# Optimization experiments

Measured on AMD Instinct MI355X. Metric: run time of the kernel, lower is better.

## Reference

```python
import math
import jax, jax.numpy as jnp
import numpy as np

B, S, DIM, H = 16, 1024, 1024, 16
HD = DIM // H            # head_dim = 64
ROPE_DIM = HD // 2       # 32; per-axis rotary dim
FT = 32                  # ft_seq_len, FT*FT == S
PT = 16                  # pt_seq_len
THETA = 10000.0
EPS = 1e-6


def _rope_cos_sin():
    # freqs_for='lang'
    freqs = 1.0 / THETA ** (jnp.arange(0, ROPE_DIM, 2, dtype=jnp.float32) / ROPE_DIM)  # [ROPE_DIM//2]
    t = jnp.arange(FT, dtype=jnp.float32) / FT * PT                                    # [FT]
    fs = jnp.einsum('n,f->nf', t, freqs)                                               # [FT, ROPE_DIM//2]
    fs = jnp.repeat(fs, 2, axis=-1)                                                    # [FT, ROPE_DIM]
    fh = jnp.broadcast_to(fs[:, None, :], (FT, FT, ROPE_DIM))
    fw = jnp.broadcast_to(fs[None, :, :], (FT, FT, ROPE_DIM))
    f = jnp.concatenate([fh, fw], axis=-1).reshape(-1, 2 * ROPE_DIM)                   # [S, HD]
    return jnp.cos(f), jnp.sin(f)


def _rotate_half(x):
    x1, x2 = jnp.split(x, 2, axis=-1)
    return jnp.concatenate((-x2, x1), axis=-1)


def _rms_norm(x, w):
    xf = x.astype(jnp.float32)
    var = jnp.mean(jnp.square(xf), axis=-1, keepdims=True)
    return (w * (xf * jax.lax.rsqrt(var + EPS))).astype(x.dtype)


def setup_inputs() -> dict:
    key = jax.random.key(0)
    ks = jax.random.split(key, 4)
    sd = 1.0 / math.sqrt(DIM)
    return {
        'x': jax.random.normal(ks[0], (B, S, DIM), dtype=jnp.float32),
        'w_qkv': jax.random.normal(ks[1], (DIM, 3 * DIM), dtype=jnp.float32) * sd,
        'b_qkv': jnp.zeros((3 * DIM,), dtype=jnp.float32),
        'q_norm_w': jnp.ones((HD,), dtype=jnp.float32),
        'k_norm_w': jnp.ones((HD,), dtype=jnp.float32),
        'w_out': jax.random.normal(ks[2], (DIM, DIM), dtype=jnp.float32) * sd,
        'b_out': jnp.zeros((DIM,), dtype=jnp.float32),
    }


def reference(x, w_qkv, b_qkv, q_norm_w, k_norm_w, w_out, b_out):
    cos, sin = _rope_cos_sin()                    # [S, HD] each
    cos = cos[None, None].astype(x.dtype)
    sin = sin[None, None].astype(x.dtype)

    qkv = x @ w_qkv + b_qkv                       # [B,S,3*DIM]
    qkv = qkv.reshape(B, S, 3, H, HD).transpose(2, 0, 3, 1, 4)  # [3,B,H,S,HD]
    q, k, v = qkv[0], qkv[1], qkv[2]

    q = _rms_norm(q, q_norm_w)
    k = _rms_norm(k, k_norm_w)

    q = q * cos + _rotate_half(q) * sin
    k = k * cos + _rotate_half(k) * sin

    scale = 1.0 / math.sqrt(HD)
    logits = jnp.einsum('bhqd,bhkd->bhqk', q.astype(jnp.float32), k.astype(jnp.float32)) * scale
    attn = jax.nn.softmax(logits, axis=-1).astype(x.dtype)
    out = jnp.einsum('bhqk,bhkd->bhqd', attn, v)  # [B,H,S,HD]

    out = out.transpose(0, 2, 1, 3).reshape(B, S, DIM)
    return out @ w_out + b_out
```

## Files before the change

kernel.cpp:

```cpp
#include <hip/hip_runtime.h>
#include <cstdint>
#include <cstddef>

#define B_    16
#define S_    1024
#define DIM_  1024
#define H_    16
#define HD_   64
#define TDIM  3072

typedef unsigned short ushort_t;
typedef unsigned int   uint_t;
typedef __attribute__((ext_vector_type(8)))  short s8v;
typedef __attribute__((ext_vector_type(4)))  float f32x4;
typedef __attribute__((ext_vector_type(16))) float f32x16;

__device__ __forceinline__ float b2f(ushort_t u) {
    union { uint_t i; float f; } t; t.i = (uint_t)u << 16; return t.f;
}
__device__ __forceinline__ ushort_t f2b(float f) {
    union { float f; uint_t i; } t; t.f = f;
    uint_t r = t.i + 0x7FFFu + ((t.i >> 16) & 1u);
    return (ushort_t)(r >> 16);
}
__device__ __forceinline__ uint_t cvt_pk_bf16(float a, float b) {
    uint_t r;
    asm("v_cvt_pk_bf16_f32 %0, %1, %2" : "=v"(r) : "v"(a), "v"(b));
    return r;
}

__device__ __forceinline__ f32x4 mfma_bf16(s8v a, s8v b, f32x4 c) {
    asm volatile("v_mfma_f32_16x16x32_bf16 %0, %1, %2, %0" : "+v"(c) : "v"(a), "v"(b));
    return c;
}
__device__ __forceinline__ f32x16 mfma32_bf16(s8v a, s8v b, f32x16 c) {
    asm volatile("v_mfma_f32_32x32x16_bf16 %0, %1, %2, %0" : "+v"(c) : "v"(a), "v"(b));
    return c;
}

__device__ __forceinline__ void gload16(const void* g, void* l) {
    __builtin_amdgcn_global_load_lds(
        (const __attribute__((address_space(1))) uint_t*)g,
        (__attribute__((address_space(3))) uint_t*)l, 16, 0, 0);
}

__device__ __forceinline__ void bar() {
    asm volatile("" ::: "memory");
    __builtin_amdgcn_s_barrier();
    asm volatile("" ::: "memory");
}
__device__ __forceinline__ void wait_vm0() {
    asm volatile("s_waitcnt vmcnt(0)" ::: "memory");
}

__global__ __launch_bounds__(256) void f32_to_bf16_vec(const float* __restrict__ src,
                                                       short* __restrict__ dst, int n8) {
    int i = blockIdx.x * 256 + threadIdx.x;
    if (i < n8) {
        float4 a = *(const float4*)(src + (size_t)i * 8);
        float4 b = *(const float4*)(src + (size_t)i * 8 + 4);
        s8v t;
        t[0] = (short)f2b(a.x); t[1] = (short)f2b(a.y);
        t[2] = (short)f2b(a.z); t[3] = (short)f2b(a.w);
        t[4] = (short)f2b(b.x); t[5] = (short)f2b(b.y);
        t[6] = (short)f2b(b.z); t[7] = (short)f2b(b.w);
        *(s8v*)(dst + (size_t)i * 8) = t;
    }
}

__global__ __launch_bounds__(256) void rope_tables(float* __restrict__ cos_t,
                                                   float* __restrict__ sin_t) {
    int idx = blockIdx.x * 256 + threadIdx.x;
    int s = idx >> 6;
    int d = idx & 63;
    int pos = (d < 32) ? (s >> 5) : (s & 31);
    int i   = (d & 31) >> 1;
    float freq  = expf(-(float)i * 0.5756462732485115f);
    float angle = (float)pos * 0.5f * freq;
    cos_t[idx] = cosf(angle);
    sin_t[idx] = sinf(angle);
}

__global__ __launch_bounds__(256) void transpose_to_bf16(const float* __restrict__ Wsrc,
                                                         short* __restrict__ WT,
                                                         int K, int N) {
    __shared__ float t[32][33];
    int tx = threadIdx.x & 31, ty = threadIdx.x >> 5;
    int n0 = blockIdx.x * 32, k0 = blockIdx.y * 32;
#pragma unroll
    for (int i = 0; i < 4; ++i)
        t[ty + 8 * i][tx] = Wsrc[(size_t)(k0 + ty + 8 * i) * N + n0 + tx];
    __syncthreads();
#pragma unroll
    for (int i = 0; i < 4; ++i)
        WT[(size_t)(n0 + ty + 8 * i) * K + k0 + tx] = (short)f2b(t[tx][ty + 8 * i]);
}

template<typename CT, bool NORM>
__global__ __launch_bounds__(512, 2) void gemm8ph(
        const short* __restrict__ A, const short* __restrict__ BT,
        const float* __restrict__ bias, CT* __restrict__ C,
        int M, int N, int K, int NX,
        const float* __restrict__ qw, const float* __restrict__ kw,
        const float* __restrict__ cos_t, const float* __restrict__ sin_t) {
    __shared__ short As[2][256 * 64];
    __shared__ short Bs[2][256 * 64];

    const int tid  = threadIdx.x;
    const int w    = tid >> 6;
    const int lane = tid & 63;
    const int l15  = lane & 15, lg = lane >> 4;
    const int wm = w >> 2, wn = w & 3;

    const int nwg  = gridDim.x;
    const int cpx  = nwg >> 3;
    const int wgid = (blockIdx.x & 7) * cpx + (blockIdx.x >> 3);
    const int bx = wgid % NX, by = wgid / NX;
    const int m0 = by * 256, n0 = bx * 256;

    const int NT = K >> 6;

    const int sgrow = w * 8 + (lane >> 3);
    const int ksrc  = (((lane & 7) ^ (lane >> 3)) * 8);

    auto stageA = [&](int t, int buf) {
        const size_t k0 = (size_t)t * 64;
#pragma unroll
        for (int j = 0; j < 4; ++j)
            gload16(A + (size_t)(m0 + j * 64 + sgrow) * K + k0 + ksrc,
                    &As[buf][(j * 64 + w * 8) * 64]);
    };
    auto stageB = [&](int t, int buf) {
        const size_t k0 = (size_t)t * 64;
#pragma unroll
        for (int j = 0; j < 4; ++j)
            gload16(BT + (size_t)(n0 + j * 64 + sgrow) * K + k0 + ksrc,
                    &Bs[buf][(j * 64 + w * 8) * 64]);
    };

    stageA(0, 0);
    stageB(0, 0);
    wait_vm0();
    bar();

    f32x4 acc[8][4] = {};
    s8v a_f[4][2];
    s8v b_f[4][2];

    const int swz = l15 & 7;

    for (int t = 0; t < NT; ++t) {
        const int buf = t & 1;
        const bool more = (t + 1 < NT);

#pragma unroll
        for (int i = 0; i < 4; ++i) {
            int row = wm * 128 + i * 16 + l15;
#pragma unroll
            for (int kk = 0; kk < 2; ++kk)
                a_f[i][kk] = *(const s8v*)&As[buf][row * 64 + (((kk * 4 + lg) ^ swz) * 8)];
        }
#pragma unroll
        for (int ni = 0; ni < 2; ++ni) {
            int row = wn * 64 + ni * 16 + l15;
#pragma unroll
            for (int kk = 0; kk < 2; ++kk)
                b_f[ni][kk] = *(const s8v*)&Bs[buf][row * 64 + (((kk * 4 + lg) ^ swz) * 8)];
        }
        if (more) stageA(t + 1, buf ^ 1);
        bar();
        __builtin_amdgcn_s_setprio(1);
#pragma unroll
        for (int i = 0; i < 4; ++i)
#pragma unroll
            for (int ni = 0; ni < 2; ++ni)
#pragma unroll
                for (int kk = 0; kk < 2; ++kk)
                    acc[i][ni] = mfma_bf16(a_f[i][kk], b_f[ni][kk], acc[i][ni]);
        __builtin_amdgcn_s_setprio(0);
        bar();

#pragma unroll
        for (int ni = 2; ni < 4; ++ni) {
            int row = wn * 64 + ni * 16 + l15;
#pragma unroll
            for (int kk = 0; kk < 2; ++kk)
                b_f[ni][kk] = *(const s8v*)&Bs[buf][row * 64 + (((kk * 4 + lg) ^ swz) * 8)];
        }
        if (more) stageB(t + 1, buf ^ 1);
        bar();
        __builtin_amdgcn_s_setprio(1);
#pragma unroll
        for (int i = 0; i < 4; ++i)
#pragma unroll
            for (int ni = 2; ni < 4; ++ni)
#pragma unroll
                for (int kk = 0; kk < 2; ++kk)
                    acc[i][ni] = mfma_bf16(a_f[i][kk], b_f[ni][kk], acc[i][ni]);
        __builtin_amdgcn_s_setprio(0);
        bar();

#pragma unroll
        for (int i = 0; i < 4; ++i) {
            int row = wm * 128 + 64 + i * 16 + l15;
#pragma unroll
            for (int kk = 0; kk < 2; ++kk)
                a_f[i][kk] = *(const s8v*)&As[buf][row * 64 + (((kk * 4 + lg) ^ swz) * 8)];
        }
        bar();
        __builtin_amdgcn_s_setprio(1);
#pragma unroll
        for (int i = 0; i < 4; ++i)
#pragma unroll
            for (int ni = 0; ni < 2; ++ni)
#pragma unroll
                for (int kk = 0; kk < 2; ++kk)
                    acc[4 + i][ni] = mfma_bf16(a_f[i][kk], b_f[ni][kk], acc[4 + i][ni]);
        __builtin_amdgcn_s_setprio(0);
        bar();

        __builtin_amdgcn_s_setprio(1);
#pragma unroll
        for (int i = 0; i < 4; ++i)
#pragma unroll
            for (int ni = 2; ni < 4; ++ni)
#pragma unroll
                for (int kk = 0; kk < 2; ++kk)
                    acc[4 + i][ni] = mfma_bf16(a_f[i][kk], b_f[ni][kk], acc[4 + i][ni]);
        __builtin_amdgcn_s_setprio(0);
        wait_vm0();
        bar();
    }

    const int colbase = n0 + wn * 64;
    if constexpr (NORM) {
        if (colbase < 2048) {
            const float* nw = (colbase < 1024) ? qw : kw;
            float wv[4], bv[4];
#pragma unroll
            for (int ni = 0; ni < 4; ++ni) {
                wv[ni] = nw[16 * ni + l15];
                bv[ni] = bias[colbase + 16 * ni + l15];
            }
#pragma unroll
            for (int mi = 0; mi < 8; ++mi) {
#pragma unroll
                for (int r = 0; r < 4; ++r) {
                    int row = m0 + wm * 128 + mi * 16 + lg * 4 + r;
                    int s = row & (S_ - 1);
                    float v[4];
#pragma unroll
                    for (int ni = 0; ni < 4; ++ni) v[ni] = acc[mi][ni][r] + bv[ni];
                    float ss = v[0]*v[0] + v[1]*v[1] + v[2]*v[2] + v[3]*v[3];
                    ss += __shfl_xor(ss, 1);
                    ss += __shfl_xor(ss, 2);
                    ss += __shfl_xor(ss, 4);
                    ss += __shfl_xor(ss, 8);
                    float rms = rsqrtf(ss * (1.0f / 64.0f) + 1e-6f);
                    float xn[4];
#pragma unroll
                    for (int ni = 0; ni < 4; ++ni) xn[ni] = v[ni] * rms * wv[ni];
#pragma unroll
                    for (int ni = 0; ni < 4; ++ni) {
                        int d = 16 * ni + l15;
                        float c  = cos_t[s * 64 + d];
                        float sn = sin_t[s * 64 + d];
                        float rot = (ni < 2) ? -xn[ni + 2] : xn[ni - 2];
                        C[(size_t)row * N + colbase + d] = (short)f2b(xn[ni] * c + rot * sn);
                    }
                }
            }
            return;
        }
    }
#pragma unroll
    for (int ni = 0; ni < 4; ++ni) {
        float bvv = bias[colbase + 16 * ni + l15];
#pragma unroll
        for (int mi = 0; mi < 8; ++mi) {
#pragma unroll
            for (int r = 0; r < 4; ++r) {
                size_t row = (size_t)(m0 + wm * 128 + mi * 16 + lg * 4 + r);
                int    col = colbase + 16 * ni + l15;
                float v = acc[mi][ni][r] + bvv;
                if constexpr (sizeof(CT) == 4) C[row * N + col] = v;
                else                           C[row * N + col] = (short)f2b(v);
            }
        }
    }
}

__global__ __launch_bounds__(256) void attn_mfma(const short* __restrict__ qkv,
                                                 short* __restrict__ attn) {
    __shared__ ushort_t pool[9216];
    ushort_t* Ks = pool;
    ushort_t* Vt = pool + 4608;

    const float SC  = 0.18033688011112042f;
    const float THR = 11.0f;

    const int tid  = threadIdx.x;
    const int w    = tid >> 6;
    const int lane = tid & 63;
    const int l31  = lane & 31, l5 = lane >> 5;

    const int bid = blockIdx.x;
    const int xcd = bid & 7;
    const int jj_ = bid >> 3;
    const int bh  = xcd * 32 + (jj_ & 31);
    const int b   = bh >> 4, h = bh & 15;
    const int q0  = (jj_ >> 5) * 128;

    const short* qbase = qkv + (size_t)b * S_ * TDIM + h * HD_;
    const short* kb_ = qbase + DIM_;
    const short* vb_ = qbase + 2 * DIM_;

    s8v qf[4];
#pragma unroll
    for (int kc = 0; kc < 4; ++kc)
        qf[kc] = *(const s8v*)(qbase + (size_t)(q0 + w * 32 + l31) * TDIM + kc * 16 + l5 * 8);

    f32x16 of0 = {}, of1 = {};
    float m_s = -1e30f, l_s = 0.f;

    const int kr   = tid >> 3;
    const int kp8  = (tid & 7) * 8;
    const int vkp  = tid >> 3;
    const int va   = tid & 7;
    const int vp8  = va * 8;
    const int vcol = (2 * vkp) ^ ((va & 3) << 4);
    const int vsw  = ((l31 >> 3) & 3) << 4;

    s8v kA, kB, vA, vB;
    auto prefetch = [&](int kt) {
        const short* kbt = kb_ + (size_t)kt * 64 * TDIM;
        const short* vbt = vb_ + (size_t)kt * 64 * TDIM;
        kA = *(const s8v*)(kbt + (size_t)kr * TDIM + kp8);
        kB = *(const s8v*)(kbt + (size_t)(kr + 32) * TDIM + kp8);
        vA = *(const s8v*)(vbt + (size_t)(2 * vkp) * TDIM + vp8);
        vB = *(const s8v*)(vbt + (size_t)(2 * vkp + 1) * TDIM + vp8);
    };
    prefetch(0);

    for (int kt = 0; kt < 16; ++kt) {
        *(s8v*)&Ks[kr * 72 + kp8]        = kA;
        *(s8v*)&Ks[(kr + 32) * 72 + kp8] = kB;
#pragma unroll
        for (int j = 0; j < 8; ++j) {
            uint_t pk = (ushort_t)vA[j] | ((uint_t)(ushort_t)vB[j] << 16);
            *(uint_t*)&Vt[(vp8 + j) * 72 + vcol] = pk;
        }
        __syncthreads();

        if (kt < 15) prefetch(kt + 1);

        f32x16 st0 = {}, st1 = {};
        __builtin_amdgcn_s_setprio(1);
#pragma unroll
        for (int kc = 0; kc < 4; ++kc) {
            s8v kf0 = *(const s8v*)&Ks[l31 * 72 + kc * 16 + l5 * 8];
            s8v kf1 = *(const s8v*)&Ks[(32 + l31) * 72 + kc * 16 + l5 * 8];
            st0 = mfma32_bf16(kf0, qf[kc], st0);
            st1 = mfma32_bf16(kf1, qf[kc], st1);
        }
        __builtin_amdgcn_s_setprio(0);

        float mx = -1e30f;
#pragma unroll
        for (int r = 0; r < 16; ++r)
            mx = fmaxf(mx, fmaxf(st0[r], st1[r]));
        mx = fmaxf(mx, __shfl_xor(mx, 32));
        float mxs = mx * SC;

        if (!__all(mxs <= m_s + THR)) {
            float mnew  = fmaxf(m_s, mxs);
            float alpha = exp2f(m_s - mnew);
            m_s = mnew;
            l_s *= alpha;
#pragma unroll
            for (int r = 0; r < 16; ++r) { of0[r] *= alpha; of1[r] *= alpha; }
        }

        float ls = 0.f;
#pragma unroll
        for (int r = 0; r < 16; ++r) {
            float p0 = exp2f(__builtin_fmaf(st0[r], SC, -m_s));
            float p1 = exp2f(__builtin_fmaf(st1[r], SC, -m_s));
            st0[r] = p0; st1[r] = p1;
            ls += p0 + p1;
        }
        ls += __shfl_xor(ls, 32);
        l_s += ls;

        uint_t P20[8], P21[8];
#pragma unroll
        for (int i = 0; i < 8; ++i) {
            P20[i] = cvt_pk_bf16(st0[2 * i], st0[2 * i + 1]);
            P21[i] = cvt_pk_bf16(st1[2 * i], st1[2 * i + 1]);
        }

#pragma unroll
        for (int kb = 0; kb < 2; ++kb) {
            const uint_t* P2 = kb ? P21 : P20;
#pragma unroll
            for (int c = 0; c < 2; ++c) {
                uint_t sw0 = __shfl_xor((int)P2[4 * c + 0], 32);
                uint_t sw1 = __shfl_xor((int)P2[4 * c + 1], 32);
                uint_t sw2 = __shfl_xor((int)P2[4 * c + 2], 32);
                uint_t sw3 = __shfl_xor((int)P2[4 * c + 3], 32);
                union { uint_t u[4]; s8v v; } pf;
                pf.u[0] = l5 ? sw2           : P2[4 * c + 0];
                pf.u[1] = l5 ? sw3           : P2[4 * c + 1];
                pf.u[2] = l5 ? P2[4 * c + 2] : sw0;
                pf.u[3] = l5 ? P2[4 * c + 3] : sw1;

                int kcol = (kb * 32 + c * 16 + l5 * 8) ^ vsw;
                s8v vf0 = *(const s8v*)&Vt[l31 * 72 + kcol];
                s8v vf1 = *(const s8v*)&Vt[(32 + l31) * 72 + kcol];
                __builtin_amdgcn_s_setprio(1);
                of0 = mfma32_bf16(vf0, pf.v, of0);
                of1 = mfma32_bf16(vf1, pf.v, of1);
                __builtin_amdgcn_s_setprio(0);
            }
        }
        __syncthreads();
    }

    float inv = 1.0f / l_s;
    ushort_t* OL = pool + w * 2304;
#pragma unroll
    for (int r = 0; r < 16; ++r) {
        int d = (r & 3) + 8 * (r >> 2) + 4 * l5;
        OL[l31 * 72 + d]      = f2b(of0[r] * inv);
        OL[l31 * 72 + 32 + d] = f2b(of1[r] * inv);
    }
#pragma unroll
    for (int i = 0; i < 4; ++i) {
        int idx = lane + i * 64;
        int row = idx >> 3, ch = idx & 7;
        *(s8v*)&attn[((size_t)b * S_ + q0 + w * 32 + row) * DIM_ + h * HD_ + ch * 8] =
            *(const s8v*)&OL[row * 72 + ch * 8];
    }
}

extern "C" void kernel_launch(void* const* d_in, const int* in_sizes, int n_in,
                              void* d_out, int out_size, void* d_ws, size_t ws_size,
                              hipStream_t stream) {
    const float* x        = (const float*)d_in[0];
    const float* w_qkv    = (const float*)d_in[1];
    const float* b_qkv    = (const float*)d_in[2];
    const float* q_norm_w = (const float*)d_in[3];
    const float* k_norm_w = (const float*)d_in[4];
    const float* w_out    = (const float*)d_in[5];
    const float* b_out    = (const float*)d_in[6];
    float* out = (float*)d_out;

    const size_t OFF_QKV = 0;
    const size_t OFF_ATT = 100663296;
    const size_t OFF_XB  = OFF_ATT + 33554432;
    const size_t OFF_WQ  = OFF_XB + 33554432;
    const size_t OFF_WO  = OFF_WQ + 6291456;
    const size_t OFF_CT  = OFF_WO + 2097152;
    const size_t OFF_ST  = OFF_CT + 262144;
    const size_t NEED    = OFF_ST + 262144;

    if (ws_size < NEED) {
        hipMemsetAsync(d_out, 0, (size_t)out_size * sizeof(float), stream);
        return;
    }

    char* ws = (char*)d_ws;
    short* qkv   = (short*)(ws + OFF_QKV);
    short* attnb = (short*)(ws + OFF_ATT);
    short* xb    = (short*)(ws + OFF_XB);
    short* wqkvT = (short*)(ws + OFF_WQ);
    short* woutT = (short*)(ws + OFF_WO);
    float* cos_t = (float*)(ws + OFF_CT);
    float* sin_t = (float*)(ws + OFF_ST);

    rope_tables<<<dim3(256), dim3(256), 0, stream>>>(cos_t, sin_t);
    f32_to_bf16_vec<<<dim3(8192), dim3(256), 0, stream>>>(x, xb, 2097152);
    transpose_to_bf16<<<dim3(96, 32), dim3(256), 0, stream>>>(w_qkv, wqkvT, 1024, 3072);
    transpose_to_bf16<<<dim3(32, 32), dim3(256), 0, stream>>>(w_out, woutT, 1024, 1024);

    gemm8ph<short, true><<<dim3(768), dim3(512), 0, stream>>>(
        xb, wqkvT, b_qkv, qkv, 16384, 3072, 1024, 12,
        q_norm_w, k_norm_w, cos_t, sin_t);

    attn_mfma<<<dim3(2048), dim3(256), 0, stream>>>(qkv, attnb);

    gemm8ph<float, false><<<dim3(256), dim3(512), 0, stream>>>(
        attnb, woutT, b_out, out, 16384, 1024, 1024, 4,
        nullptr, nullptr, nullptr, nullptr);
}
```

Measured before the change: 319.8 us.

## Permute V^T key columns so P accumulators feed MFMA directly without shuffles

The V tile is written transposed into LDS with a permuted key-column order that matches the MFMA accumulator layout of P. This lets the PV MFMA take P fragments straight from registers and drops the cross-lane shuffles and selects. The row max now uses v_max3 in two parallel chains, the exp-sum uses four independent accumulators, and the priority raise is hoisted around the whole PV loop. The change depends on the permutation matching the 32x32 MFMA output layout exactly, so any mismatch would produce wrong results.

Measured after the change: 318.5 us. No clear change (-0.4%).

```diff
diff --git a/kernel.cpp b/kernel.cpp
--- a/kernel.cpp
+++ b/kernel.cpp
@@ -26,6 +26,11 @@
 __device__ __forceinline__ uint_t cvt_pk_bf16(float a, float b) {
     uint_t r;
     asm("v_cvt_pk_bf16_f32 %0, %1, %2" : "=v"(r) : "v"(a), "v"(b));
+    return r;
+}
+__device__ __forceinline__ float max3f(float a, float b, float c) {
+    float r;
+    asm("v_max3_f32 %0, %1, %2, %3" : "=v"(r) : "v"(a), "v"(b), "v"(c));
     return r;
 }
 
@@ -328,8 +333,10 @@
     const int vkp  = tid >> 3;
     const int va   = tid & 7;
     const int vp8  = va * 8;
-    const int vcol = (2 * vkp) ^ ((va & 3) << 4);
-    const int vsw  = ((l31 >> 3) & 3) << 4;
+    const int k2    = 2 * vkp;
+    const int kperm = (k2 & 0x33) | ((k2 & 4) << 1) | ((k2 & 8) >> 1);
+    const int vcol  = kperm ^ ((va & 3) << 4);
+    const int vsw   = ((l31 >> 3) & 3) << 4;
 
     s8v kA, kB, vA, vB;
     auto prefetch = [&](int kt) {
@@ -337,8 +344,8 @@
         const short* vbt = vb_ + (size_t)kt * 64 * TDIM;
         kA = *(const s8v*)(kbt + (size_t)kr * TDIM + kp8);
         kB = *(const s8v*)(kbt + (size_t)(kr + 32) * TDIM + kp8);
-        vA = *(const s8v*)(vbt + (size_t)(2 * vkp) * TDIM + vp8);
-        vB = *(const s8v*)(vbt + (size_t)(2 * vkp + 1) * TDIM + vp8);
+        vA = *(const s8v*)(vbt + (size_t)k2 * TDIM + vp8);
+        vB = *(const s8v*)(vbt + (size_t)(k2 + 1) * TDIM + vp8);
     };
     prefetch(0);
 
@@ -365,10 +372,14 @@
         }
         __builtin_amdgcn_s_setprio(0);
 
-        float mx = -1e30f;
-#pragma unroll
-        for (int r = 0; r < 16; ++r)
-            mx = fmaxf(mx, fmaxf(st0[r], st1[r]));
+        float ma = fmaxf(st0[0], st1[0]);
+        float mb = fmaxf(st0[8], st1[8]);
+#pragma unroll
+        for (int r = 1; r < 8; ++r) {
+            ma = max3f(st0[r],     st1[r],     ma);
+            mb = max3f(st0[8 + r], st1[8 + r], mb);
+        }
+        float mx = fmaxf(ma, mb);
         mx = fmaxf(mx, __shfl_xor(mx, 32));
         float mxs = mx * SC;
 
@@ -381,14 +392,18 @@
             for (int r = 0; r < 16; ++r) { of0[r] *= alpha; of1[r] *= alpha; }
         }
 
-        float ls = 0.f;
-#pragma unroll
-        for (int r = 0; r < 16; ++r) {
-            float p0 = exp2f(__builtin_fmaf(st0[r], SC, -m_s));
-            float p1 = exp2f(__builtin_fmaf(st1[r], SC, -m_s));
-            st0[r] = p0; st1[r] = p1;
-            ls += p0 + p1;
-        }
+        float la = 0.f, lb = 0.f, lc = 0.f, ld = 0.f;
+#pragma unroll
+        for (int r = 0; r < 16; r += 2) {
+            float p00 = exp2f(__builtin_fmaf(st0[r],     SC, -m_s));
+            float p01 = exp2f(__builtin_fmaf(st0[r + 1], SC, -m_s));
+            float p10 = exp2f(__builtin_fmaf(st1[r],     SC, -m_s));
+            float p11 = exp2f(__builtin_fmaf(st1[r + 1], SC, -m_s));
+            st0[r] = p00; st0[r + 1] = p01;
+            st1[r] = p10; st1[r + 1] = p11;
+            la += p00; lb += p01; lc += p10; ld += p11;
+        }
+        float ls = (la + lb) + (lc + ld);
         ls += __shfl_xor(ls, 32);
         l_s += ls;
 
@@ -399,30 +414,26 @@
             P21[i] = cvt_pk_bf16(st1[2 * i], st1[2 * i + 1]);
         }
 
+        __builtin_amdgcn_s_setprio(1);
 #pragma unroll
         for (int kb = 0; kb < 2; ++kb) {
             const uint_t* P2 = kb ? P21 : P20;
 #pragma unroll
             for (int c = 0; c < 2; ++c) {
-                uint_t sw0 = __shfl_xor((int)P2[4 * c + 0], 32);
-                uint_t sw1 = __shfl_xor((int)P2[4 * c + 1], 32);
-                uint_t sw2 = __shfl_xor((int)P2[4 * c + 2], 32);
-                uint_t sw3 = __shfl_xor((int)P2[4 * c + 3], 32);
                 union { uint_t u[4]; s8v v; } pf;
-                pf.u[0] = l5 ? sw2           : P2[4 * c + 0];
-                pf.u[1] = l5 ? sw3           : P2[4 * c + 1];
-                pf.u[2] = l5 ? P2[4 * c + 2] : sw0;
-                pf.u[3] = l5 ? P2[4 * c + 3] : sw1;
+                pf.u[0] = P2[4 * c + 0];
+                pf.u[1] = P2[4 * c + 1];
+                pf.u[2] = P2[4 * c + 2];
+                pf.u[3] = P2[4 * c + 3];
 
                 int kcol = (kb * 32 + c * 16 + l5 * 8) ^ vsw;
                 s8v vf0 = *(const s8v*)&Vt[l31 * 72 + kcol];
                 s8v vf1 = *(const s8v*)&Vt[(32 + l31) * 72 + kcol];
-                __builtin_amdgcn_s_setprio(1);
                 of0 = mfma32_bf16(vf0, pf.v, of0);
                 of1 = mfma32_bf16(vf1, pf.v, of1);
-                __builtin_amdgcn_s_setprio(0);
             }
         }
+        __builtin_amdgcn_s_setprio(0);
         __syncthreads();
     }
 
```
